# Performance work log

Measured on AMD Instinct MI355X. Metric: run time of the kernel, lower is better.

Reference implementation:

```python
import jax, jax.numpy as jnp
import numpy as np

EMB_DIM = 2048
NHEADS = 16
KVHEADS = 4
D_KQ = 128
D_V = 128


def setup_inputs() -> dict:
    key = jax.random.key(0)
    ks = jax.random.split(key, 7)
    B, S = 2, 2048
    std = 0.02
    return {
        "q": jax.random.normal(ks[0], (B, S, EMB_DIM), jnp.float32),
        "k": jax.random.normal(ks[1], (B, S, EMB_DIM), jnp.float32),
        "v": jax.random.normal(ks[2], (B, S, EMB_DIM), jnp.float32),
        # weights stored [in, out] (transposed vs torch nn.Linear storage)
        "Wq": jax.random.normal(ks[3], (EMB_DIM, NHEADS * D_KQ), jnp.float32) * std,
        "Wk": jax.random.normal(ks[4], (EMB_DIM, KVHEADS * D_KQ), jnp.float32) * std,
        "Wv": jax.random.normal(ks[5], (EMB_DIM, KVHEADS * D_V), jnp.float32) * std,
        "Wo": jax.random.normal(ks[6], (NHEADS * D_V, EMB_DIM), jnp.float32) * std,
    }


def reference(q, k, v, Wq, Wk, Wv, Wo):
    B, S, _ = q.shape
    scale = D_KQ ** -0.25  # applied to both q and k -> combined 1/sqrt(d_kq)
    # per-head projections: [B, H, S, d]
    qh = (q @ Wq).reshape(B, S, NHEADS, D_KQ).transpose(0, 2, 1, 3) * scale
    kh = (k @ Wk).reshape(B, S, KVHEADS, D_KQ).transpose(0, 2, 1, 3) * scale
    vh = (v @ Wv).reshape(B, S, KVHEADS, D_V).transpose(0, 2, 1, 3)
    # GQA expansion: each kv head repeated `expansion` times consecutively
    expansion = NHEADS // KVHEADS
    kh = jnp.repeat(kh, expansion, axis=1)  # [B, H, S, d_kq]
    vh = jnp.repeat(vh, expansion, axis=1)  # [B, H, S, d_v]
    # full softmax FIRST, then causal tril mask, then renormalize (source quirk)
    scores = jax.nn.softmax(jnp.einsum("bhqd,bhkd->bhqk", qh, kh), axis=-1)
    scores = jnp.tril(scores)  # zero out strictly-upper triangle on last 2 dims
    scores = scores / (jnp.sum(scores, axis=-1, keepdims=True) + 1e-9)
    qkv = jnp.einsum("bhqk,bhkd->bhqd", scores, vh)  # [B, H, S, d_v]
    z = qkv.transpose(0, 2, 1, 3).reshape(B, S, NHEADS * D_V)
    return z @ Wo
```

## Files before the change

### kernel.cpp

```cpp
#include <hip/hip_runtime.h>

#define S_LEN 2048
#define EMB 2048
#define NH 16
#define KVH 4
#define DH 128

typedef __bf16 bf16x8 __attribute__((ext_vector_type(8)));
typedef float floatx4 __attribute__((ext_vector_type(4)));
typedef unsigned short ushortx8 __attribute__((ext_vector_type(8)));
typedef unsigned short ushortx4 __attribute__((ext_vector_type(4)));

static __device__ __forceinline__ unsigned short f2bf(float f) {
  unsigned u = __float_as_uint(f);
  return (unsigned short)((u + 0x7fffu + ((u >> 16) & 1u)) >> 16);
}

static __device__ __forceinline__ void gload16(const unsigned short* g, unsigned short* l) {
  __builtin_amdgcn_global_load_lds(
      (const __attribute__((address_space(1))) unsigned int*)(const void*)g,
      (__attribute__((address_space(3))) unsigned int*)(void*)l, 16, 0, 0);
}

__global__ __launch_bounds__(256) void pre_kernel(
    const float* __restrict__ q, const float* __restrict__ k, const float* __restrict__ v,
    const float* __restrict__ Wq, const float* __restrict__ Wk,
    const float* __restrict__ Wv, const float* __restrict__ Wo,
    unsigned short* __restrict__ qo, unsigned short* __restrict__ ko,
    unsigned short* __restrict__ vo,
    unsigned short* __restrict__ Wqt, unsigned short* __restrict__ Wkt,
    unsigned short* __restrict__ Wvt, unsigned short* __restrict__ Wot,
    float scale) {
  __shared__ float t[32][33];
  int bx = blockIdx.x;
  if (bx < 12288) {
    const int sel = bx >> 12;
    const float* in = (sel == 0) ? q : (sel == 1) ? k : v;
    unsigned short* out = (sel == 0) ? qo : (sel == 1) ? ko : vo;
    size_t i = (((size_t)(bx & 4095)) * 256 + threadIdx.x) * 8;
    floatx4 a = *(const floatx4*)(in + i);
    floatx4 bvec = *(const floatx4*)(in + i + 4);
    ushortx8 o;
    #pragma unroll
    for (int c = 0; c < 4; ++c) { o[c] = f2bf(a[c]); o[4 + c] = f2bf(bvec[c]); }
    *(ushortx8*)(out + i) = o;
  } else {
    bx -= 12288;
    const float* W; unsigned short* Wt; int N, tile; float sc;
    if (bx < 4096)      { W = Wq; Wt = Wqt; N = 2048; tile = bx;        sc = scale; }
    else if (bx < 5120) { W = Wk; Wt = Wkt; N = 512;  tile = bx - 4096; sc = scale; }
    else if (bx < 6144) { W = Wv; Wt = Wvt; N = 512;  tile = bx - 5120; sc = 1.0f; }
    else                { W = Wo; Wt = Wot; N = 2048; tile = bx - 6144; sc = 1.0f; }
    const int ntiles = N >> 5;
    const int n0 = (tile % ntiles) * 32, k0 = (tile / ntiles) * 32;
    const int tx = threadIdx.x & 31, ty = threadIdx.x >> 5;
    #pragma unroll
    for (int r = 0; r < 4; ++r)
      t[ty + r * 8][tx] = W[(size_t)(k0 + ty + r * 8) * N + n0 + tx];
    __syncthreads();
    #pragma unroll
    for (int r = 0; r < 4; ++r)
      Wt[(size_t)(n0 + ty + r * 8) * 2048 + k0 + tx] = f2bf(t[tx][ty + r * 8] * sc);
  }
}

static __device__ __forceinline__ void gemm256_core(
    const unsigned short* __restrict__ Ab, const unsigned short* __restrict__ Bb,
    bool swap, unsigned short* As, unsigned short* Bs, floatx4 (&acc)[8][4]) {
  const int tid = threadIdx.x;
  const int lane = tid & 63, w = tid >> 6;
  const int lm = lane & 15, gq = lane >> 4;
  const int wm = w >> 2, wn = w & 3;
  const int lr = lane >> 3, lc = (lane & 7) ^ lr;

  auto stageH = [&](const unsigned short* gb, unsigned short* lt, int half, int kst) {
    #pragma unroll
    for (int qq = 0; qq < 2; ++qq) {
      const int rb = half * 128 + w * 16 + qq * 8;
      gload16(gb + (((size_t)(rb + lr)) << 11) + kst + (lc << 3), lt + rb * 64);
    }
  };

  unsigned short* As2 = As + 16384;
  unsigned short* Bs2 = Bs + 16384;

  stageH(Ab, As, 0, 0);  stageH(Ab, As, 1, 0);
  stageH(Bb, Bs, 0, 0);  stageH(Bb, Bs, 1, 0);
  stageH(Ab, As2, 0, 64);
  asm volatile("s_waitcnt vmcnt(2)" ::: "memory");
  __builtin_amdgcn_s_barrier();

  const int r1 = (wm * 128 + lm) * 64;
  const int r2 = (wn * 64 + lm) * 64;
  const int c0 = ((0 + gq) ^ (lm & 7)) * 8;
  const int c1 = ((4 + gq) ^ (lm & 7)) * 8;

#define TILE_BODY(CA, CB, OA, OB, KS1, KS2, STG1, STG4)                                         \
  {                                                                                             \
    const unsigned short* l1 = swap ? (CB) : (CA);                                              \
    const unsigned short* l2 = swap ? (CA) : (CB);                                              \
    bf16x8 op1[8], o2a[4], o2b[4];                                                              \
    _Pragma("unroll") for (int i = 0; i < 8; ++i)                                               \
      op1[i] = *(const bf16x8*)&l1[r1 + i * 1024 + c0];                                         \
    _Pragma("unroll") for (int j = 0; j < 4; ++j)                                               \
      o2a[j] = *(const bf16x8*)&l2[r2 + j * 1024 + c0];                                         \
    if (STG1) stageH(Ab, (OA), 1, (KS1));                                                       \
    __builtin_amdgcn_s_barrier();                                                               \
    asm volatile("s_waitcnt lgkmcnt(0)" ::: "memory");                                          \
    __builtin_amdgcn_s_setprio(1);                                                              \
    _Pragma("unroll") for (int i = 0; i < 8; ++i) {                                             \
      acc[i][0] = __builtin_amdgcn_mfma_f32_16x16x32_bf16(op1[i], o2a[0], acc[i][0], 0, 0, 0);  \
      acc[i][1] = __builtin_amdgcn_mfma_f32_16x16x32_bf16(op1[i], o2a[1], acc[i][1], 0, 0, 0);  \
    }                                                                                           \
    __builtin_amdgcn_s_setprio(0);                                                              \
    __builtin_amdgcn_s_barrier();                                                               \
    _Pragma("unroll") for (int j = 0; j < 4; ++j)                                               \
      o2b[j] = *(const bf16x8*)&l2[r2 + j * 1024 + c1];                                         \
    if (STG1) stageH(Bb, (OB), 0, (KS1));                                                       \
    __builtin_amdgcn_s_barrier();                                                               \
    asm volatile("s_waitcnt lgkmcnt(0)" ::: "memory");                                          \
    __builtin_amdgcn_s_setprio(1);                                                              \
    _Pragma("unroll") for (int i = 0; i < 8; ++i) {                                             \
      acc[i][2] = __builtin_amdgcn_mfma_f32_16x16x32_bf16(op1[i], o2a[2], acc[i][2], 0, 0, 0);  \
      acc[i][3] = __builtin_amdgcn_mfma_f32_16x16x32_bf16(op1[i], o2a[3], acc[i][3], 0, 0, 0);  \
    }                                                                                           \
    __builtin_amdgcn_s_setprio(0);                                                               \
    __builtin_amdgcn_s_barrier();                                                               \
    _Pragma("unroll") for (int i = 0; i < 8; ++i)                                               \
      op1[i] = *(const bf16x8*)&l1[r1 + i * 1024 + c1];                                         \
    if (STG1) stageH(Bb, (OB), 1, (KS1));                                                       \
    __builtin_amdgcn_s_barrier();                                                               \
    asm volatile("s_waitcnt lgkmcnt(0)" ::: "memory");                                          \
    __builtin_amdgcn_s_setprio(1);                                                              \
    _Pragma("unroll") for (int i = 0; i < 8; ++i) {                                             \
      acc[i][0] = __builtin_amdgcn_mfma_f32_16x16x32_bf16(op1[i], o2b[0], acc[i][0], 0, 0, 0);  \
      acc[i][1] = __builtin_amdgcn_mfma_f32_16x16x32_bf16(op1[i], o2b[1], acc[i][1], 0, 0, 0);  \
    }                                                                                           \
    __builtin_amdgcn_s_setprio(0);                                                               \
    __builtin_amdgcn_s_barrier();                                                               \
    if (STG4) stageH(Ab, (CA), 0, (KS2));                                                       \
    __builtin_amdgcn_s_barrier();                                                               \
    __builtin_amdgcn_s_setprio(1);                                                              \
    _Pragma("unroll") for (int i = 0; i < 8; ++i) {                                             \
      acc[i][2] = __builtin_amdgcn_mfma_f32_16x16x32_bf16(op1[i], o2b[2], acc[i][2], 0, 0, 0);  \
      acc[i][3] = __builtin_amdgcn_mfma_f32_16x16x32_bf16(op1[i], o2b[3], acc[i][3], 0, 0, 0);  \
    }                                                                                           \
    __builtin_amdgcn_s_setprio(0);                                                               \
    if (STG4) { asm volatile("s_waitcnt vmcnt(2)" ::: "memory"); }                              \
    else      { asm volatile("s_waitcnt vmcnt(0)" ::: "memory"); }                              \
    __builtin_amdgcn_s_barrier();                                                               \
  }

  #pragma unroll 1
  for (int t = 0; t < 30; t += 2) {
    TILE_BODY(As, Bs, As2, Bs2, (t + 1) * 64, (t + 2) * 64, 1, 1);
    TILE_BODY(As2, Bs2, As, Bs, (t + 2) * 64, (t + 3) * 64, 1, 1);
  }
  TILE_BODY(As, Bs, As2, Bs2, 31 * 64, 0, 1, 0);
  TILE_BODY(As2, Bs2, As, Bs, 0, 0, 0, 0);
#undef TILE_BODY
}

__global__ __launch_bounds__(512, 2) void proj_kernel(
    const unsigned short* __restrict__ qb, const unsigned short* __restrict__ kb,
    const unsigned short* __restrict__ vb,
    const unsigned short* __restrict__ Wqt, const unsigned short* __restrict__ Wkt,
    const unsigned short* __restrict__ Wvt,
    unsigned short* __restrict__ Qh, unsigned short* __restrict__ Kh,
    unsigned short* __restrict__ Vt) {
  extern __shared__ unsigned short lds[];
  unsigned short* As = lds;
  unsigned short* Bs = lds + 32768;
  int bid = (int)blockIdx.x;
  bid = (bid & 7) * 24 + (bid >> 3);
  const unsigned short *Ab, *Bb;
  int task, bn, bt;
  if (bid < 128)      { task = 0; bn = bid >> 4;         bt = bid & 15;         Ab = qb; Bb = Wqt; }
  else if (bid < 160) { task = 1; bn = (bid - 128) >> 4; bt = (bid - 128) & 15; Ab = kb; Bb = Wkt; }
  else                { task = 2; bn = (bid - 160) >> 4; bt = (bid - 160) & 15; Ab = vb; Bb = Wvt; }
  Ab += ((size_t)bt) << 19;
  Bb += ((size_t)bn) << 19;

  floatx4 acc[8][4] = {};
  gemm256_core(Ab, Bb, task != 2, As, Bs, acc);

  const int tid = threadIdx.x, lane = tid & 63, w = tid >> 6;
  const int lm = lane & 15, gq = lane >> 4;
  const int wm = w >> 2, wn = w & 3;
  if (task != 2) {
    unsigned short* outp = (task == 0) ? Qh : Kh;
    const int nheads = (task == 0) ? NH : KVH;
    const int head = bn * 2 + wm;
    #pragma unroll
    for (int i = 0; i < 8; ++i) {
      const int d0 = i * 16 + gq * 4;
      #pragma unroll
      for (int j = 0; j < 4; ++j) {
        const int tg = bt * 256 + wn * 64 + j * 16 + lm;
        const int b_ = tg >> 11, s_ = tg & 2047;
        ushortx4 pk;
        #pragma unroll
        for (int r = 0; r < 4; ++r) pk[r] = f2bf(acc[i][j][r]);
        *(ushortx4*)&outp[((size_t)(b_ * nheads + head) * S_LEN + s_) * DH + d0] = pk;
      }
    }
  } else {
    #pragma unroll
    for (int i = 0; i < 8; ++i) {
      const int sgl = bt * 256 + wm * 128 + i * 16 + gq * 4;
      const int b_ = sgl >> 11, s_ = sgl & 2047;
      #pragma unroll
      for (int j = 0; j < 4; ++j) {
        const int dl = wn * 64 + j * 16;
        const int head = bn * 2 + (dl >> 7);
        const int dd = (dl & 127) + lm;
        ushortx4 pk;
        #pragma unroll
        for (int r = 0; r < 4; ++r) pk[r] = f2bf(acc[i][j][r]);
        *(ushortx4*)&Vt[((size_t)(b_ * KVH + head) * DH + dd) * S_LEN + s_] = pk;
      }
    }
  }
}

__global__ __launch_bounds__(512, 2) void out_kernel(const unsigned short* __restrict__ Z,
                                                     const unsigned short* __restrict__ Wot,
                                                     float* __restrict__ outp) {
  extern __shared__ unsigned short lds[];
  unsigned short* As = lds;
  unsigned short* Bs = lds + 32768;
  int bid = (int)blockIdx.x;
  bid = (bid & 7) * 16 + (bid >> 3);
  const int bn = bid >> 4, bt = bid & 15;

  floatx4 acc[8][4] = {};
  gemm256_core(Z + (((size_t)bt) << 19), Wot + (((size_t)bn) << 19), true, As, Bs, acc);

  const int tid = threadIdx.x, lane = tid & 63, w = tid >> 6;
  const int lm = lane & 15, gq = lane >> 4;
  const int wm = w >> 2, wn = w & 3;
  #pragma unroll
  for (int i = 0; i < 8; ++i) {
    const int n0 = bn * 256 + wm * 128 + i * 16 + gq * 4;
    #pragma unroll
    for (int j = 0; j < 4; ++j) {
      const int tg = bt * 256 + wn * 64 + j * 16 + lm;
      *(floatx4*)&outp[(size_t)tg * 2048 + n0] = acc[i][j];
    }
  }
}

__global__ __launch_bounds__(256, 2) void attn_kernel(const unsigned short* __restrict__ Qh,
                                                      const unsigned short* __restrict__ Kh,
                                                      const unsigned short* __restrict__ Vt,
                                                      unsigned short* __restrict__ Z) {
  extern __shared__ unsigned short alds[];
  unsigned short* KsB = alds;
  unsigned short* VsB = alds + 16384;
  unsigned short* PsB = alds + 32768;
  const int tid = threadIdx.x;
  const int w = tid >> 6, lane = tid & 63;
  const int lm = lane & 15, gq = lane >> 4;
  const int h = blockIdx.y, b = blockIdx.z;
  const int qt = b ? (15 - (int)blockIdx.x) : (int)blockIdx.x;
  const unsigned short* Kp = Kh + (size_t)(b * KVH + (h >> 2)) * S_LEN * DH;
  const unsigned short* Vp = Vt + (size_t)(b * KVH + (h >> 2)) * DH * S_LEN;
  unsigned short* psW = PsB + w * (32 * 64);

  const int krr = w * 16 + (lane >> 4);
  const int kcE = ((lane & 15) ^ (lane >> 4)) * 8;
  const int kcO = ((lane & 15) ^ ((lane >> 4) | 4)) * 8;
  auto loadK = [&](int kv, unsigned short* dstbuf) {
    #pragma unroll
    for (int i = 0; i < 4; ++i)
      gload16(Kp + (size_t)(kv + krr + i * 4) * DH + ((i & 1) ? kcO : kcE),
              dstbuf + w * 2048 + i * 512);
  };
  const int vrow8 = tid >> 3;
  const int vsig = (tid & 7) ^ (vrow8 & 7);
  const unsigned short* vsrc0 = Vp + (size_t)vrow8 * S_LEN + vsig * 8;
  auto loadV = [&](int kv, unsigned short* dstbuf) {
    unsigned short* dst = dstbuf + w * 512;
    #pragma unroll
    for (int i = 0; i < 4; ++i)
      gload16(vsrc0 + (size_t)(i * 32) * S_LEN + kv, dst + i * 2048);
  };

  int kcol[4];
  #pragma unroll
  for (int kk = 0; kk < 4; ++kk) kcol[kk] = ((kk * 4 + gq) ^ (lm & 7)) * 8;
  const int sw0 = (gq ^ (lm & 7)) * 8;
  const int sw1 = ((4 | gq) ^ (lm & 7)) * 8;

  bf16x8 ones;
  #pragma unroll
  for (int c = 0; c < 8; ++c) ones[c] = (__bf16)1.0f;

  const int Q0 = qt * 128;
  const int nit = 2 * qt + 2;
  const unsigned short* Qp = Qh + ((size_t)(b * NH + h) * S_LEN + Q0) * DH;

  loadK(0, KsB);
  loadV(0, VsB);
  bf16x8 qfr[2][4];
  #pragma unroll
  for (int g = 0; g < 2; ++g)
    #pragma unroll
    for (int kk = 0; kk < 4; ++kk)
      qfr[g][kk] = *(const bf16x8*)(Qp + (size_t)(w * 32 + g * 16 + lm) * DH + kk * 32 + gq * 8);
  asm volatile("s_waitcnt vmcnt(0)" ::: "memory");
  __builtin_amdgcn_s_barrier();
  int buf = 0;

  floatx4 acc_o[2][8] = {};
  floatx4 acc_l[2] = {};

  #pragma unroll 1
  for (int it = 0; it < nit; ++it) {
    const int kv0 = it * 64;
    const unsigned short* Kc = KsB + buf * 8192;
    const unsigned short* Vc = VsB + buf * 8192;
    if (it + 1 < nit) {
      loadK(kv0 + 64, KsB + (buf ^ 1) * 8192);
      loadV(kv0 + 64, VsB + (buf ^ 1) * 8192);
    }
    bf16x8 kreg[4][4];
    #pragma unroll
    for (int j = 0; j < 4; ++j)
      #pragma unroll
      for (int kk = 0; kk < 4; ++kk)
        kreg[j][kk] = *(const bf16x8*)&Kc[(j * 16 + lm) * 128 + kcol[kk]];
    floatx4 sa[2][4] = {};
    #pragma unroll
    for (int g = 0; g < 2; ++g)
      #pragma unroll
      for (int j = 0; j < 4; ++j)
        #pragma unroll
        for (int kk = 0; kk < 4; ++kk)
          sa[g][j] = __builtin_amdgcn_mfma_f32_16x16x32_bf16(qfr[g][kk], kreg[j][kk], sa[g][j], 0, 0, 0);
    #pragma unroll
    for (int g = 0; g < 2; ++g) {
      const int rowb = Q0 + w * 32 + g * 16 + gq * 4;
      #pragma unroll
      for (int r = 0; r < 4; ++r) {
        const int qg = rowb + r;
        const int prow = g * 16 + gq * 4 + r;
        #pragma unroll
        for (int j = 0; j < 4; ++j) {
          const int kg = kv0 + j * 16 + lm;
          const float p = (kg <= qg) ? __expf(sa[g][j][r]) : 0.0f;
          const int pcol = j * 16 + lm;
          psW[prow * 64 + (((pcol >> 3) ^ (prow & 7)) << 3) + (pcol & 7)] =
              __builtin_bit_cast(unsigned short, (__bf16)p);
        }
      }
    }
    bf16x8 ap[2][2];
    #pragma unroll
    for (int g = 0; g < 2; ++g) {
      const int rrow = g * 16 + lm;
      ap[g][0] = *(const bf16x8*)&psW[rrow * 64 + ((gq ^ (rrow & 7)) << 3)];
      ap[g][1] = *(const bf16x8*)&psW[rrow * 64 + (((4 | gq) ^ (rrow & 7)) << 3)];
    }
    #pragma unroll
    for (int jd = 0; jd < 8; ++jd) {
      const int row = (jd * 16 + lm) * 64;
      bf16x8 bv0 = *(const bf16x8*)&Vc[row + sw0];
      bf16x8 bv1 = *(const bf16x8*)&Vc[row + sw1];
      #pragma unroll
      for (int g = 0; g < 2; ++g) {
        acc_o[g][jd] = __builtin_amdgcn_mfma_f32_16x16x32_bf16(bv0, ap[g][0], acc_o[g][jd], 0, 0, 0);
        acc_o[g][jd] = __builtin_amdgcn_mfma_f32_16x16x32_bf16(bv1, ap[g][1], acc_o[g][jd], 0, 0, 0);
      }
    }
    #pragma unroll
    for (int g = 0; g < 2; ++g) {
      acc_l[g] = __builtin_amdgcn_mfma_f32_16x16x32_bf16(ones, ap[g][0], acc_l[g], 0, 0, 0);
      acc_l[g] = __builtin_amdgcn_mfma_f32_16x16x32_bf16(ones, ap[g][1], acc_l[g], 0, 0, 0);
    }
    asm volatile("s_waitcnt vmcnt(0) lgkmcnt(0)" ::: "memory");
    __builtin_amdgcn_s_barrier();
    buf ^= 1;
  }

  #pragma unroll
  for (int g = 0; g < 2; ++g) {
    const float inv = 1.0f / acc_l[g][0];
    const size_t t_ = (size_t)b * S_LEN + Q0 + w * 32 + g * 16 + lm;
    #pragma unroll
    for (int jd = 0; jd < 8; ++jd) {
      ushortx4 pk;
      #pragma unroll
      for (int r = 0; r < 4; ++r) pk[r] = f2bf(acc_o[g][jd][r] * inv);
      *(ushortx4*)&Z[t_ * (NH * DH) + h * DH + jd * 16 + gq * 4] = pk;
    }
  }
}

extern "C" void kernel_launch(void* const* d_in, const int* in_sizes, int n_in,
                              void* d_out, int out_size, void* d_ws, size_t ws_size,
                              hipStream_t stream) {
  (void)in_sizes; (void)n_in; (void)out_size; (void)ws_size;
  const float* q  = (const float*)d_in[0];
  const float* k  = (const float*)d_in[1];
  const float* v  = (const float*)d_in[2];
  const float* Wq = (const float*)d_in[3];
  const float* Wk = (const float*)d_in[4];
  const float* Wv = (const float*)d_in[5];
  const float* Wo = (const float*)d_in[6];

  unsigned short* Qh  = (unsigned short*)d_ws;
  unsigned short* Kh  = Qh + (size_t)2 * NH * S_LEN * DH;
  unsigned short* Vt  = Kh + (size_t)2 * KVH * S_LEN * DH;
  unsigned short* Z   = Vt + (size_t)2 * KVH * S_LEN * DH;
  unsigned short* vb  = Z + (size_t)4096 * 2048;
  unsigned short* Wqt = vb + (size_t)4096 * 2048;
  unsigned short* Wkt = Wqt + (size_t)2048 * 2048;
  unsigned short* Wvt = Wkt + (size_t)512 * 2048;
  unsigned short* Wot = Wvt + (size_t)512 * 2048;
  unsigned short* qb = (unsigned short*)d_out;
  unsigned short* kb = qb + (size_t)4096 * 2048;

  const float scale = 0.29730177875068026f;

  static int s_attr_done = 0;
  if (!s_attr_done) {
    hipFuncSetAttribute(reinterpret_cast<const void*>(proj_kernel),
                        hipFuncAttributeMaxDynamicSharedMemorySize, 131072);
    hipFuncSetAttribute(reinterpret_cast<const void*>(out_kernel),
                        hipFuncAttributeMaxDynamicSharedMemorySize, 131072);
    hipFuncSetAttribute(reinterpret_cast<const void*>(attn_kernel),
                        hipFuncAttributeMaxDynamicSharedMemorySize, 81920);
    s_attr_done = 1;
  }

  pre_kernel<<<22528, 256, 0, stream>>>(q, k, v, Wq, Wk, Wv, Wo,
                                        qb, kb, vb, Wqt, Wkt, Wvt, Wot, scale);
  proj_kernel<<<192, 512, 131072, stream>>>(qb, kb, vb, Wqt, Wkt, Wvt, Qh, Kh, Vt);
  attn_kernel<<<dim3(16, 16, 2), 256, 81920, stream>>>(Qh, Kh, Vt, Z);
  out_kernel<<<128, 512, 131072, stream>>>(Z, Wot, (float*)d_out);
}
```

Measured before the change: 347.5 us.

## Split KV tiles across wave halves and pair causal q-tiles per attention block

The attention kernel now runs 512 threads per block. The two groups of four waves each handle half of a 128-wide KV tile, and their partial output and row-sum accumulators are combined through shared memory at the end. Each block processes two query tiles in sequence, one long and one short (15-x and x), which balances causal work across blocks and halves the grid. This raises per-block parallelism and balances the load, but it needs 144KB of LDS, which likely allows only one block per CU, and it adds a reduction step and extra barriers.

After: 335.2 us. 1.04x faster.

```diff
diff --git a/kernel.cpp b/kernel.cpp
--- a/kernel.cpp
+++ b/kernel.cpp
@@ -250,150 +250,161 @@
   }
 }
 
-__global__ __launch_bounds__(256, 2) void attn_kernel(const unsigned short* __restrict__ Qh,
+__global__ __launch_bounds__(512, 2) void attn_kernel(const unsigned short* __restrict__ Qh,
                                                       const unsigned short* __restrict__ Kh,
                                                       const unsigned short* __restrict__ Vt,
                                                       unsigned short* __restrict__ Z) {
   extern __shared__ unsigned short alds[];
   unsigned short* KsB = alds;
-  unsigned short* VsB = alds + 16384;
-  unsigned short* PsB = alds + 32768;
+  unsigned short* VsB = alds + 32768;
+  unsigned short* PsB = alds + 65536;
   const int tid = threadIdx.x;
   const int w = tid >> 6, lane = tid & 63;
+  const int wlo = w & 3, whi = w >> 2;
   const int lm = lane & 15, gq = lane >> 4;
   const int h = blockIdx.y, b = blockIdx.z;
-  const int qt = b ? (15 - (int)blockIdx.x) : (int)blockIdx.x;
   const unsigned short* Kp = Kh + (size_t)(b * KVH + (h >> 2)) * S_LEN * DH;
   const unsigned short* Vp = Vt + (size_t)(b * KVH + (h >> 2)) * DH * S_LEN;
-  unsigned short* psW = PsB + w * (32 * 64);
-
-  const int krr = w * 16 + (lane >> 4);
-  const int kcE = ((lane & 15) ^ (lane >> 4)) * 8;
-  const int kcO = ((lane & 15) ^ ((lane >> 4) | 4)) * 8;
-  auto loadK = [&](int kv, unsigned short* dstbuf) {
+  unsigned short* psW = PsB + w * (16 * 64);
+
+  const int dr = lane >> 4;
+  const int srcswz = ((lane & 15) ^ ((w * 4 + dr) & 7)) * 8;
+  auto loadK = [&](int kv, int bsel) {
+    unsigned short* dst = KsB + bsel * 16384 + w * 512;
     #pragma unroll
     for (int i = 0; i < 4; ++i)
-      gload16(Kp + (size_t)(kv + krr + i * 4) * DH + ((i & 1) ? kcO : kcE),
-              dstbuf + w * 2048 + i * 512);
+      gload16(Kp + (size_t)(kv + i * 32 + w * 4 + dr) * DH + srcswz, dst + i * 4096);
   };
-  const int vrow8 = tid >> 3;
-  const int vsig = (tid & 7) ^ (vrow8 & 7);
-  const unsigned short* vsrc0 = Vp + (size_t)vrow8 * S_LEN + vsig * 8;
-  auto loadV = [&](int kv, unsigned short* dstbuf) {
-    unsigned short* dst = dstbuf + w * 512;
+  auto loadV = [&](int kv, int bsel) {
+    unsigned short* dst = VsB + bsel * 16384 + w * 512;
     #pragma unroll
     for (int i = 0; i < 4; ++i)
-      gload16(vsrc0 + (size_t)(i * 32) * S_LEN + kv, dst + i * 2048);
+      gload16(Vp + (size_t)(i * 32 + w * 4 + dr) * S_LEN + kv + srcswz, dst + i * 4096);
   };
 
   int kcol[4];
   #pragma unroll
   for (int kk = 0; kk < 4; ++kk) kcol[kk] = ((kk * 4 + gq) ^ (lm & 7)) * 8;
-  const int sw0 = (gq ^ (lm & 7)) * 8;
-  const int sw1 = ((4 | gq) ^ (lm & 7)) * 8;
+  const int sw0 = (whi * 8 + (gq ^ (lm & 7))) * 8;
+  const int sw1 = (whi * 8 + ((4 | gq) ^ (lm & 7))) * 8;
 
   bf16x8 ones;
   #pragma unroll
   for (int c = 0; c < 8; ++c) ones[c] = (__bf16)1.0f;
 
-  const int Q0 = qt * 128;
-  const int nit = 2 * qt + 2;
-  const unsigned short* Qp = Qh + ((size_t)(b * NH + h) * S_LEN + Q0) * DH;
-
-  loadK(0, KsB);
-  loadV(0, VsB);
-  bf16x8 qfr[2][4];
-  #pragma unroll
-  for (int g = 0; g < 2; ++g)
-    #pragma unroll
-    for (int kk = 0; kk < 4; ++kk)
-      qfr[g][kk] = *(const bf16x8*)(Qp + (size_t)(w * 32 + g * 16 + lm) * DH + kk * 32 + gq * 8);
-  asm volatile("s_waitcnt vmcnt(0)" ::: "memory");
-  __builtin_amdgcn_s_barrier();
-  int buf = 0;
-
-  floatx4 acc_o[2][8] = {};
-  floatx4 acc_l[2] = {};
-
   #pragma unroll 1
-  for (int it = 0; it < nit; ++it) {
-    const int kv0 = it * 64;
-    const unsigned short* Kc = KsB + buf * 8192;
-    const unsigned short* Vc = VsB + buf * 8192;
-    if (it + 1 < nit) {
-      loadK(kv0 + 64, KsB + (buf ^ 1) * 8192);
-      loadV(kv0 + 64, VsB + (buf ^ 1) * 8192);
-    }
-    bf16x8 kreg[4][4];
-    #pragma unroll
-    for (int j = 0; j < 4; ++j)
+  for (int pass = 0; pass < 2; ++pass) {
+    const int qt = pass ? (int)blockIdx.x : 15 - (int)blockIdx.x;
+    const int Q0 = qt * 128;
+    const int nit = qt + 1;
+    const unsigned short* Qp = Qh + ((size_t)(b * NH + h) * S_LEN + Q0) * DH;
+    bf16x8 qfr[2][4];
+    #pragma unroll
+    for (int g = 0; g < 2; ++g)
       #pragma unroll
       for (int kk = 0; kk < 4; ++kk)
-        kreg[j][kk] = *(const bf16x8*)&Kc[(j * 16 + lm) * 128 + kcol[kk]];
-    floatx4 sa[2][4] = {};
-    #pragma unroll
-    for (int g = 0; g < 2; ++g)
+        qfr[g][kk] = *(const bf16x8*)(Qp + (size_t)(wlo * 32 + g * 16 + lm) * DH + kk * 32 + gq * 8);
+
+    floatx4 acc_o[2][8] = {};
+    floatx4 acc_l[2] = {};
+
+    loadK(0, 0);
+    loadV(0, 0);
+    asm volatile("s_waitcnt vmcnt(0)" ::: "memory");
+    __builtin_amdgcn_s_barrier();
+    int buf = 0;
+
+    #pragma unroll 1
+    for (int it = 0; it < nit; ++it) {
+      const int kv0 = it * 128;
+      const unsigned short* Kc = KsB + buf * 16384 + (whi * 64) * 128;
+      const unsigned short* Vc = VsB + buf * 16384;
+      if (it + 1 < nit) { loadK(kv0 + 128, buf ^ 1); loadV(kv0 + 128, buf ^ 1); }
+      bf16x8 kreg[4][4];
       #pragma unroll
       for (int j = 0; j < 4; ++j)
         #pragma unroll
         for (int kk = 0; kk < 4; ++kk)
-          sa[g][j] = __builtin_amdgcn_mfma_f32_16x16x32_bf16(qfr[g][kk], kreg[j][kk], sa[g][j], 0, 0, 0);
-    #pragma unroll
-    for (int g = 0; g < 2; ++g) {
-      const int rowb = Q0 + w * 32 + g * 16 + gq * 4;
-      #pragma unroll
-      for (int r = 0; r < 4; ++r) {
-        const int qg = rowb + r;
-        const int prow = g * 16 + gq * 4 + r;
-        #pragma unroll
-        for (int j = 0; j < 4; ++j) {
-          const int kg = kv0 + j * 16 + lm;
-          const float p = (kg <= qg) ? __expf(sa[g][j][r]) : 0.0f;
-          const int pcol = j * 16 + lm;
-          psW[prow * 64 + (((pcol >> 3) ^ (prow & 7)) << 3) + (pcol & 7)] =
-              __builtin_bit_cast(unsigned short, (__bf16)p);
+          kreg[j][kk] = *(const bf16x8*)&Kc[(j * 16 + lm) * 128 + kcol[kk]];
+      floatx4 sa[2][4] = {};
+      #pragma unroll
+      for (int g = 0; g < 2; ++g)
+        #pragma unroll
+        for (int j = 0; j < 4; ++j)
+          #pragma unroll
+          for (int kk = 0; kk < 4; ++kk)
+            sa[g][j] = __builtin_amdgcn_mfma_f32_16x16x32_bf16(qfr[g][kk], kreg[j][kk], sa[g][j], 0, 0, 0);
+      bf16x8 ap[2][2];
+      #pragma unroll
+      for (int g = 0; g < 2; ++g) {
+        const int rowb = Q0 + wlo * 32 + g * 16 + gq * 4;
+        #pragma unroll
+        for (int r = 0; r < 4; ++r) {
+          const int qg = rowb + r;
+          const int prow = gq * 4 + r;
+          #pragma unroll
+          for (int j = 0; j < 4; ++j) {
+            const int kg = kv0 + whi * 64 + j * 16 + lm;
+            const float p = (kg <= qg) ? __expf(sa[g][j][r]) : 0.0f;
+            const int pcol = j * 16 + lm;
+            psW[prow * 64 + (((pcol >> 3) ^ (prow & 7)) << 3) + (pcol & 7)] =
+                __builtin_bit_cast(unsigned short, (__bf16)p);
+          }
         }
-      }
-    }
-    bf16x8 ap[2][2];
-    #pragma unroll
-    for (int g = 0; g < 2; ++g) {
-      const int rrow = g * 16 + lm;
-      ap[g][0] = *(const bf16x8*)&psW[rrow * 64 + ((gq ^ (rrow & 7)) << 3)];
-      ap[g][1] = *(const bf16x8*)&psW[rrow * 64 + (((4 | gq) ^ (rrow & 7)) << 3)];
-    }
-    #pragma unroll
-    for (int jd = 0; jd < 8; ++jd) {
-      const int row = (jd * 16 + lm) * 64;
-      bf16x8 bv0 = *(const bf16x8*)&Vc[row + sw0];
-      bf16x8 bv1 = *(const bf16x8*)&Vc[row + sw1];
+        ap[g][0] = *(const bf16x8*)&psW[lm * 64 + ((gq ^ (lm & 7)) << 3)];
+        ap[g][1] = *(const bf16x8*)&psW[lm * 64 + (((4 | gq) ^ (lm & 7)) << 3)];
+      }
+      #pragma unroll
+      for (int jd = 0; jd < 8; ++jd) {
+        const int row = (jd * 16 + lm) * 128;
+        bf16x8 bv0 = *(const bf16x8*)&Vc[row + sw0];
+        bf16x8 bv1 = *(const bf16x8*)&Vc[row + sw1];
+        #pragma unroll
+        for (int g = 0; g < 2; ++g) {
+          acc_o[g][jd] = __builtin_amdgcn_mfma_f32_16x16x32_bf16(bv0, ap[g][0], acc_o[g][jd], 0, 0, 0);
+          acc_o[g][jd] = __builtin_amdgcn_mfma_f32_16x16x32_bf16(bv1, ap[g][1], acc_o[g][jd], 0, 0, 0);
+        }
+      }
       #pragma unroll
       for (int g = 0; g < 2; ++g) {
-        acc_o[g][jd] = __builtin_amdgcn_mfma_f32_16x16x32_bf16(bv0, ap[g][0], acc_o[g][jd], 0, 0, 0);
-        acc_o[g][jd] = __builtin_amdgcn_mfma_f32_16x16x32_bf16(bv1, ap[g][1], acc_o[g][jd], 0, 0, 0);
-      }
-    }
-    #pragma unroll
-    for (int g = 0; g < 2; ++g) {
-      acc_l[g] = __builtin_amdgcn_mfma_f32_16x16x32_bf16(ones, ap[g][0], acc_l[g], 0, 0, 0);
-      acc_l[g] = __builtin_amdgcn_mfma_f32_16x16x32_bf16(ones, ap[g][1], acc_l[g], 0, 0, 0);
-    }
-    asm volatile("s_waitcnt vmcnt(0) lgkmcnt(0)" ::: "memory");
-    __builtin_amdgcn_s_barrier();
-    buf ^= 1;
-  }
-
-  #pragma unroll
-  for (int g = 0; g < 2; ++g) {
-    const float inv = 1.0f / acc_l[g][0];
-    const size_t t_ = (size_t)b * S_LEN + Q0 + w * 32 + g * 16 + lm;
-    #pragma unroll
-    for (int jd = 0; jd < 8; ++jd) {
-      ushortx4 pk;
-      #pragma unroll
-      for (int r = 0; r < 4; ++r) pk[r] = f2bf(acc_o[g][jd][r] * inv);
-      *(ushortx4*)&Z[t_ * (NH * DH) + h * DH + jd * 16 + gq * 4] = pk;
-    }
+        acc_l[g] = __builtin_amdgcn_mfma_f32_16x16x32_bf16(ones, ap[g][0], acc_l[g], 0, 0, 0);
+        acc_l[g] = __builtin_amdgcn_mfma_f32_16x16x32_bf16(ones, ap[g][1], acc_l[g], 0, 0, 0);
+      }
+      asm volatile("s_waitcnt vmcnt(0) lgkmcnt(0)" ::: "memory");
+      __builtin_amdgcn_s_barrier();
+      buf ^= 1;
+    }
+
+    float* scO = (float*)KsB;
+    float* scL = (float*)VsB;
+    if (whi == 1) {
+      #pragma unroll
+      for (int g = 0; g < 2; ++g) {
+        #pragma unroll
+        for (int jd = 0; jd < 8; ++jd)
+          #pragma unroll
+          for (int r = 0; r < 4; ++r)
+            scO[wlo * 4096 + (g * 32 + jd * 4 + r) * 64 + lane] = acc_o[g][jd][r];
+        scL[wlo * 128 + g * 64 + lane] = acc_l[g][0];
+      }
+    }
+    __syncthreads();
+    if (whi == 0) {
+      #pragma unroll
+      for (int g = 0; g < 2; ++g) {
+        const float inv = 1.0f / (acc_l[g][0] + scL[wlo * 128 + g * 64 + lane]);
+        const size_t t_ = (size_t)b * S_LEN + Q0 + wlo * 32 + g * 16 + lm;
+        #pragma unroll
+        for (int jd = 0; jd < 8; ++jd) {
+          ushortx4 pk;
+          #pragma unroll
+          for (int r = 0; r < 4; ++r)
+            pk[r] = f2bf((acc_o[g][jd][r] + scO[wlo * 4096 + (g * 32 + jd * 4 + r) * 64 + lane]) * inv);
+          *(ushortx4*)&Z[t_ * (NH * DH) + h * DH + jd * 16 + gq * 4] = pk;
+        }
+      }
+    }
+    __syncthreads();
   }
 }
 
@@ -430,13 +441,13 @@
     hipFuncSetAttribute(reinterpret_cast<const void*>(out_kernel),
                         hipFuncAttributeMaxDynamicSharedMemorySize, 131072);
     hipFuncSetAttribute(reinterpret_cast<const void*>(attn_kernel),
-                        hipFuncAttributeMaxDynamicSharedMemorySize, 81920);
+                        hipFuncAttributeMaxDynamicSharedMemorySize, 147456);
     s_attr_done = 1;
   }
 
   pre_kernel<<<22528, 256, 0, stream>>>(q, k, v, Wq, Wk, Wv, Wo,
                                         qb, kb, vb, Wqt, Wkt, Wvt, Wot, scale);
   proj_kernel<<<192, 512, 131072, stream>>>(qb, kb, vb, Wqt, Wkt, Wvt, Qh, Kh, Vt);
-  attn_kernel<<<dim3(16, 16, 2), 256, 81920, stream>>>(Qh, Kh, Vt, Z);
+  attn_kernel<<<dim3(8, 16, 2), 512, 147456, stream>>>(Qh, Kh, Vt, Z);
   out_kernel<<<128, 512, 131072, stream>>>(Z, Wot, (float*)d_out);
 }
```
